# Performance work log

Hardware: AMD Instinct MI355X
Metric: run time of the kernel (lower is better)

## Reference

```python
import jax, jax.numpy as jnp
import numpy as np

E, NH, G = 2048, 16, 4
HD = E // NH          # head_dim = 128
KV = E // G           # kv proj width = 512 == G * HD
B, S = 2, 2048


def setup_inputs() -> dict:
    key = jax.random.key(0)
    ks = jax.random.split(key, 7)
    s = lambda n: 1.0 / np.sqrt(n)
    return {
        "query": jax.random.normal(ks[0], (B, S, E), jnp.float32),
        "key_in": jax.random.normal(ks[1], (B, S, E), jnp.float32),
        "value": jax.random.normal(ks[2], (B, S, E), jnp.float32),
        "Wq": jax.random.normal(ks[3], (E, E), jnp.float32) * s(E),
        "bq": jnp.zeros((E,), jnp.float32),
        "Wk": jax.random.normal(ks[4], (E, KV), jnp.float32) * s(E),
        "bk": jnp.zeros((KV,), jnp.float32),
        "Wv": jax.random.normal(ks[5], (E, KV), jnp.float32) * s(E),
        "bv": jnp.zeros((KV,), jnp.float32),
        "Wo": jax.random.normal(ks[6], (E, E), jnp.float32) * s(E),
        "bo": jnp.zeros((E,), jnp.float32),
    }


def reference(query, key_in, value, Wq, bq, Wk, bk, Wv, bv, Wo, bo):
    b, s, _ = query.shape
    scale = HD ** -0.5
    # projections
    q = (query @ Wq + bq).reshape(b, s, NH, HD).transpose(0, 2, 1, 3)   # [B,NH,S,HD]
    k = (key_in @ Wk + bk).reshape(b, s, G, HD).transpose(0, 2, 1, 3)   # [B,G,S,HD]
    v = (value @ Wv + bv).reshape(b, s, G, HD).transpose(0, 2, 1, 3)    # [B,G,S,HD]
    # grouped-query attention: each KV head serves NH//G query heads
    qg = q.reshape(b, G, NH // G, s, HD)                                # [B,G,NH/G,S,HD]
    scores = jnp.einsum('bgqsh,bgth->bgqst', qg, k) * scale             # [B,G,NH/G,S,S]
    w = jax.nn.softmax(scores, axis=-1)
    out = jnp.einsum('bgqst,bgth->bgqsh', w, v)                         # [B,G,NH/G,S,HD]
    out = out.reshape(b, NH, s, HD).transpose(0, 2, 1, 3).reshape(b, s, E)
    return out @ Wo + bo
```

## Files before the change

### kernel.cpp

```cpp
#include <hip/hip_runtime.h>
#include <hip/hip_bf16.h>

#define E_ 2048
#define S_ 2048
#define B_ 2
#define BS_ 4096
#define KV_ 512
#define NH_ 16
#define G_ 4
#define HD_ 128
#define QK_SCALE 0.08838834764831845f
#define LOG2E_ 1.4426950408889634f

typedef __attribute__((ext_vector_type(8))) short short8;
typedef __attribute__((ext_vector_type(4))) float floatx4;
typedef __attribute__((ext_vector_type(4))) unsigned short ushort4_;

static __device__ __forceinline__ unsigned short f2bf(float f) {
  unsigned int u = __builtin_bit_cast(unsigned int, f);
  u += 0x7fffu + ((u >> 16) & 1u);
  return (unsigned short)(u >> 16);
}

static __device__ __forceinline__ unsigned int cvt_pk_bf16(float lo, float hi) {
  unsigned int r;
  asm("v_cvt_pk_bf16_f32 %0, %1, %2" : "=v"(r) : "v"(lo), "v"(hi));
  return r;
}

static __device__ __forceinline__ void gld16(const void* g, void* l) {
  __builtin_amdgcn_global_load_lds(
      (const __attribute__((address_space(1))) unsigned int*)g,
      (__attribute__((address_space(3))) unsigned int*)l, 16, 0, 0);
}

__global__ __launch_bounds__(256) void k_prep(
    const float* __restrict__ q, const float* __restrict__ k, const float* __restrict__ v,
    unsigned short* __restrict__ xq, unsigned short* __restrict__ xk,
    unsigned short* __restrict__ xv,
    const float* __restrict__ Wq, unsigned short* __restrict__ WqT,
    const float* __restrict__ Wk, unsigned short* __restrict__ WkT,
    const float* __restrict__ Wv, unsigned short* __restrict__ WvT,
    const float* __restrict__ Wo, unsigned short* __restrict__ WoT) {
  __shared__ float ts[32][33];
  int bid = blockIdx.x;
  if (bid < 24576) {
    int which = bid >> 13;
    int i = (bid & 8191) * 256 + threadIdx.x;
    const float* in = (which == 0) ? q : (which == 1) ? k : v;
    unsigned short* out = (which == 0) ? xq : (which == 1) ? xk : xv;
    float4 vv = reinterpret_cast<const float4*>(in)[i];
    ushort4_ o;
    o.x = f2bf(vv.x); o.y = f2bf(vv.y); o.z = f2bf(vv.z); o.w = f2bf(vv.w);
    reinterpret_cast<ushort4_*>(out)[i] = o;
    return;
  }
  int t = bid - 24576;
  const float* in; unsigned short* out; int N; int rem;
  if (t < 4096)      { in = Wq; out = WqT; N = 2048; rem = t; }
  else if (t < 5120) { in = Wk; out = WkT; N = 512;  rem = t - 4096; }
  else if (t < 6144) { in = Wv; out = WvT; N = 512;  rem = t - 5120; }
  else               { in = Wo; out = WoT; N = 2048; rem = t - 6144; }
  const int K = 2048;
  int nx = N >> 5;
  int bx = rem % nx, by = rem / nx;
  int tx = threadIdx.x & 31, ty = threadIdx.x >> 5;
  int n0 = bx * 32, k0 = by * 32;
#pragma unroll
  for (int i = 0; i < 4; ++i)
    ts[ty + i * 8][tx] = in[(size_t)(k0 + ty + i * 8) * N + n0 + tx];
  __syncthreads();
#pragma unroll
  for (int i = 0; i < 4; ++i)
    out[(size_t)(n0 + ty + i * 8) * K + k0 + tx] = f2bf(ts[tx][ty + i * 8]);
}

template <bool OUT_F32>
static __device__ __forceinline__ void gemm_bt_tile(
    const unsigned short* __restrict__ A, const unsigned short* __restrict__ Bt,
    const float* __restrict__ bias, bool rowBias, void* __restrict__ C,
    int N, int K, float scale, int bx, int by,
    unsigned short* As, unsigned short* Bs) {
  const int tid = threadIdx.x;
  const int w = tid >> 6;
  const int lhi = (tid >> 4) & 3;
  const int llo = tid & 15;
  const int wr = w >> 1, wc = w & 1;
  const size_t brow = (size_t)by * 128, bcol = (size_t)bx * 128;

  auto stage = [&](int k0, int bufi) {
#pragma unroll
    for (int i = 0; i < 2; ++i) {
      int o = i * 256 + tid;
      gld16(A + (brow + (o >> 2)) * K + k0 + (o & 3) * 8,
            As + bufi * 4096 + (size_t)(i * 256 + w * 64) * 8);
      gld16(Bt + (bcol + (o >> 2)) * K + k0 + (o & 3) * 8,
            Bs + bufi * 4096 + (size_t)(i * 256 + w * 64) * 8);
    }
  };

  floatx4 acc[4][4];
#pragma unroll
  for (int i = 0; i < 4; ++i)
#pragma unroll
    for (int j = 0; j < 4; ++j)
      acc[i][j] = (floatx4){0.f, 0.f, 0.f, 0.f};

  stage(0, 0);
  __syncthreads();
  int buf = 0;
  const int nk = K >> 5;
  for (int t = 0; t < nk; ++t) {
    if (t + 1 < nk) stage((t + 1) * 32, buf ^ 1);
    const unsigned short* Ab = As + buf * 4096;
    const unsigned short* Bb = Bs + buf * 4096;
    short8 a[4], b[4];
#pragma unroll
    for (int f = 0; f < 4; ++f) {
      a[f] = *reinterpret_cast<const short8*>(Ab + (wr * 64 + f * 16 + llo) * 32 + lhi * 8);
      b[f] = *reinterpret_cast<const short8*>(Bb + (wc * 64 + f * 16 + llo) * 32 + lhi * 8);
    }
    __builtin_amdgcn_s_setprio(1);
#pragma unroll
    for (int i = 0; i < 4; ++i)
#pragma unroll
      for (int j = 0; j < 4; ++j)
        acc[i][j] = __builtin_amdgcn_mfma_f32_16x16x32_bf16(a[i], b[j], acc[i][j], 0, 0, 0);
    __builtin_amdgcn_s_setprio(0);
    __syncthreads();
    buf ^= 1;
  }

#pragma unroll
  for (int i = 0; i < 4; ++i) {
#pragma unroll
    for (int j = 0; j < 4; ++j) {
      size_t gr0 = brow + wr * 64 + i * 16 + lhi * 4;
      size_t gc = bcol + wc * 64 + j * 16 + llo;
#pragma unroll
      for (int r = 0; r < 4; ++r) {
        size_t grow = gr0 + r;
        float v = acc[i][j][r];
        v += rowBias ? bias[grow] : bias[gc];
        v *= scale;
        if (OUT_F32)
          ((float*)C)[grow * N + gc] = v;
        else
          ((unsigned short*)C)[grow * N + gc] = f2bf(v);
      }
    }
  }
}

__global__ __launch_bounds__(256) void k_gemm_qkv(
    const unsigned short* __restrict__ xq, const unsigned short* __restrict__ WqT,
    const float* __restrict__ bq, unsigned short* __restrict__ qb,
    const unsigned short* __restrict__ xk, const unsigned short* __restrict__ WkT,
    const float* __restrict__ bk, unsigned short* __restrict__ kb,
    const unsigned short* __restrict__ WvT, const unsigned short* __restrict__ xv,
    const float* __restrict__ bv, unsigned short* __restrict__ vtb) {
  __shared__ __align__(16) unsigned short As[2 * 128 * 32];
  __shared__ __align__(16) unsigned short Bs[2 * 128 * 32];
  int bid = blockIdx.x;
  if (bid < 512) {
    int cm = (bid & 7) * 64 + (bid >> 3);
    gemm_bt_tile<false>(xq, WqT, bq, false, qb, E_, E_, QK_SCALE * LOG2E_,
                        cm >> 5, cm & 31, As, Bs);
  } else if (bid < 640) {
    int u = bid - 512;
    int cm = (u & 7) * 16 + (u >> 3);
    gemm_bt_tile<false>(xk, WkT, bk, false, kb, KV_, E_, 1.0f, cm >> 5, cm & 31, As, Bs);
  } else {
    int u = bid - 640;
    int cm = (u & 7) * 16 + (u >> 3);
    gemm_bt_tile<false>(WvT, xv, bv, true, vtb, BS_, E_, 1.0f, cm >> 2, cm & 3, As, Bs);
  }
}

__global__ __launch_bounds__(256) void k_gemm_o(
    const unsigned short* __restrict__ A, const unsigned short* __restrict__ Bt,
    const float* __restrict__ bias, float* __restrict__ C) {
  __shared__ __align__(16) unsigned short As[2 * 128 * 32];
  __shared__ __align__(16) unsigned short Bs[2 * 128 * 32];
  int cm = (blockIdx.x & 7) * 64 + (blockIdx.x >> 3);
  gemm_bt_tile<true>(A, Bt, bias, false, C, E_, E_, 1.0f, cm >> 5, cm & 31, As, Bs);
}

__global__ __launch_bounds__(512) void k_attn(
    const unsigned short* __restrict__ qb, const unsigned short* __restrict__ kb,
    const unsigned short* __restrict__ vt, unsigned short* __restrict__ attn) {
  __shared__ __align__(16) unsigned short Ks[2][64 * 128];
  __shared__ __align__(16) unsigned short Vs[2][128 * 64];
  __shared__ __align__(16) unsigned short Ps[8][32 * 64];

  const int tid = threadIdx.x;
  const int w = tid >> 6;
  const int lhi = (tid >> 4) & 3;
  const int llo = tid & 15;
  const int bid = blockIdx.x;
  const int xcd = bid & 7;
  const int b = xcd >> 2, g = xcd & 3;
  const int inner = bid >> 3;
  const int hq = inner & 3, qt = inner >> 2;
  const int h = g * 4 + hq;

  char* PsW = (char*)&Ps[0][0] + w * 4096;

  short8 qf[2][4];
#pragma unroll
  for (int rt = 0; rt < 2; ++rt)
#pragma unroll
    for (int hc = 0; hc < 4; ++hc) {
      int row = qt * 256 + w * 32 + rt * 16 + llo;
      qf[rt][hc] = *reinterpret_cast<const short8*>(
          qb + ((size_t)(b * 2048 + row)) * 2048 + h * 128 + hc * 32 + lhi * 8);
    }

  floatx4 acc[2][8];
#pragma unroll
  for (int rt = 0; rt < 2; ++rt)
#pragma unroll
    for (int dc = 0; dc < 8; ++dc)
      acc[rt][dc] = (floatx4){0.f, 0.f, 0.f, 0.f};
  float m_[2] = {-1e30f, -1e30f};
  float l_[2] = {0.f, 0.f};

  auto stage = [&](int kv0, int buf) {
#pragma unroll
    for (int i = 0; i < 2; ++i) {
      int o = i * 512 + tid;
      int row = o >> 4, gr2 = (o & 15) ^ (row & 7);
      gld16(kb + ((size_t)(b * 2048 + kv0 + row)) * 512 + g * 128 + gr2 * 8,
            &Ks[buf][(size_t)(i * 512 + w * 64) * 8]);
    }
#pragma unroll
    for (int i = 0; i < 2; ++i) {
      int o = i * 512 + tid;
      int row = o >> 3, gr2 = (o & 7) ^ (row & 7);
      gld16(vt + ((size_t)(g * 128 + row)) * 4096 + b * 2048 + kv0 + gr2 * 8,
            &Vs[buf][(size_t)(i * 512 + w * 64) * 8]);
    }
  };

  stage(0, 0);
  __syncthreads();
  int buf = 0;

  for (int t = 0; t < 32; ++t) {
    const int kv0 = t * 64;
    if (t < 31) stage(kv0 + 64, buf ^ 1);

    floatx4 sc[2][4];
#pragma unroll
    for (int rt = 0; rt < 2; ++rt)
#pragma unroll
      for (int c = 0; c < 4; ++c)
        sc[rt][c] = (floatx4){0.f, 0.f, 0.f, 0.f};
    __builtin_amdgcn_s_setprio(1);
#pragma unroll
    for (int c = 0; c < 4; ++c) {
      int krow = c * 16 + llo;
#pragma unroll
      for (int hc = 0; hc < 4; ++hc) {
        int byteoff = krow * 256 + ((hc * 64 + lhi * 16) ^ ((krow & 7) << 4));
        short8 kf = *reinterpret_cast<const short8*>((const char*)&Ks[buf][0] + byteoff);
        sc[0][c] = __builtin_amdgcn_mfma_f32_16x16x32_bf16(kf, qf[0][hc], sc[0][c], 0, 0, 0);
        sc[1][c] = __builtin_amdgcn_mfma_f32_16x16x32_bf16(kf, qf[1][hc], sc[1][c], 0, 0, 0);
      }
    }
    __builtin_amdgcn_s_setprio(0);

#pragma unroll
    for (int rt = 0; rt < 2; ++rt) {
      float pm = sc[rt][0][0];
#pragma unroll
      for (int c = 0; c < 4; ++c)
#pragma unroll
        for (int r = 0; r < 4; ++r) pm = fmaxf(pm, sc[rt][c][r]);
      if (__any(pm > m_[rt] + 8.0f)) {
        float t2 = pm;
        t2 = fmaxf(t2, __shfl_xor(t2, 16));
        t2 = fmaxf(t2, __shfl_xor(t2, 32));
        float m2 = fmaxf(m_[rt], t2);
        float scr = __builtin_amdgcn_exp2f(m_[rt] - m2);
        m_[rt] = m2;
        l_[rt] *= scr;
#pragma unroll
        for (int r = 0; r < 4; ++r) {
          float s_r = __shfl(scr, (tid & 48) | (((tid >> 2) & 12) + r));
#pragma unroll
          for (int dc = 0; dc < 8; ++dc) acc[rt][dc][r] *= s_r;
        }
      }
      float lsum = l_[rt];
#pragma unroll
      for (int c = 0; c < 4; ++c) {
        float e0 = __builtin_amdgcn_exp2f(sc[rt][c][0] - m_[rt]);
        float e1 = __builtin_amdgcn_exp2f(sc[rt][c][1] - m_[rt]);
        float e2 = __builtin_amdgcn_exp2f(sc[rt][c][2] - m_[rt]);
        float e3 = __builtin_amdgcn_exp2f(sc[rt][c][3] - m_[rt]);
        lsum += (e0 + e1) + (e2 + e3);
        uint2 pk;
        pk.x = cvt_pk_bf16(e0, e1);
        pk.y = cvt_pk_bf16(e2, e3);
        int byteoff = (rt * 16 + llo) * 128 + ((c * 32 + lhi * 8) ^ ((llo & 7) << 4));
        *reinterpret_cast<uint2*>(PsW + byteoff) = pk;
      }
      l_[rt] = lsum;
    }

    short8 pf[2][2];
#pragma unroll
    for (int rt = 0; rt < 2; ++rt)
#pragma unroll
      for (int kc = 0; kc < 2; ++kc) {
        int byteoff = (rt * 16 + llo) * 128 + ((kc * 64 + lhi * 16) ^ ((llo & 7) << 4));
        pf[rt][kc] = *reinterpret_cast<const short8*>(PsW + byteoff);
      }
    __builtin_amdgcn_s_setprio(1);
#pragma unroll
    for (int dc = 0; dc < 8; ++dc) {
      int vrow = dc * 16 + llo;
      int bo0 = vrow * 128 + ((lhi * 16) ^ ((vrow & 7) << 4));
      int bo1 = vrow * 128 + ((64 + lhi * 16) ^ ((vrow & 7) << 4));
      short8 vf0 = *reinterpret_cast<const short8*>((const char*)&Vs[buf][0] + bo0);
      short8 vf1 = *reinterpret_cast<const short8*>((const char*)&Vs[buf][0] + bo1);
      acc[0][dc] = __builtin_amdgcn_mfma_f32_16x16x32_bf16(pf[0][0], vf0, acc[0][dc], 0, 0, 0);
      acc[1][dc] = __builtin_amdgcn_mfma_f32_16x16x32_bf16(pf[1][0], vf0, acc[1][dc], 0, 0, 0);
      acc[0][dc] = __builtin_amdgcn_mfma_f32_16x16x32_bf16(pf[0][1], vf1, acc[0][dc], 0, 0, 0);
      acc[1][dc] = __builtin_amdgcn_mfma_f32_16x16x32_bf16(pf[1][1], vf1, acc[1][dc], 0, 0, 0);
    }
    __builtin_amdgcn_s_setprio(0);
    __syncthreads();
    buf ^= 1;
  }

#pragma unroll
  for (int rt = 0; rt < 2; ++rt) {
    float t2 = l_[rt];
    t2 += __shfl_xor(t2, 16);
    t2 += __shfl_xor(t2, 32);
    float linv = 1.0f / t2;
    float lr[4];
#pragma unroll
    for (int r = 0; r < 4; ++r)
      lr[r] = __shfl(linv, (tid & 48) | (((tid >> 2) & 12) + r));
#pragma unroll
    for (int dc = 0; dc < 8; ++dc)
#pragma unroll
      for (int r = 0; r < 4; ++r) {
        int row = qt * 256 + w * 32 + rt * 16 + lhi * 4 + r;
        float v = acc[rt][dc][r] * lr[r];
        attn[((size_t)(b * 2048 + row)) * 2048 + h * 128 + dc * 16 + llo] = f2bf(v);
      }
  }
}

extern "C" void kernel_launch(void* const* d_in, const int* in_sizes, int n_in,
                              void* d_out, int out_size, void* d_ws, size_t ws_size,
                              hipStream_t stream) {
  const float* query  = (const float*)d_in[0];
  const float* key_in = (const float*)d_in[1];
  const float* value  = (const float*)d_in[2];
  const float* Wq = (const float*)d_in[3];
  const float* bq = (const float*)d_in[4];
  const float* Wk = (const float*)d_in[5];
  const float* bk = (const float*)d_in[6];
  const float* Wv = (const float*)d_in[7];
  const float* bv = (const float*)d_in[8];
  const float* Wo = (const float*)d_in[9];
  const float* bo = (const float*)d_in[10];
  float* out = (float*)d_out;

  char* ws = (char*)d_ws;
  size_t off = 0;
  auto alloc = [&](size_t bytes) {
    char* p = ws + off;
    off += (bytes + 255) & ~(size_t)255;
    return p;
  };
  unsigned short* xq   = (unsigned short*)alloc((size_t)BS_ * E_ * 2);
  unsigned short* xk   = (unsigned short*)alloc((size_t)BS_ * E_ * 2);
  unsigned short* xv   = (unsigned short*)alloc((size_t)BS_ * E_ * 2);
  unsigned short* WqT  = (unsigned short*)alloc((size_t)E_ * E_ * 2);
  unsigned short* WkT  = (unsigned short*)alloc((size_t)KV_ * E_ * 2);
  unsigned short* WvT  = (unsigned short*)alloc((size_t)KV_ * E_ * 2);
  unsigned short* WoT  = (unsigned short*)alloc((size_t)E_ * E_ * 2);
  unsigned short* qb   = (unsigned short*)alloc((size_t)BS_ * E_ * 2);
  unsigned short* kb   = (unsigned short*)alloc((size_t)BS_ * KV_ * 2);
  unsigned short* vtb  = (unsigned short*)alloc((size_t)KV_ * BS_ * 2);
  unsigned short* attb = (unsigned short*)alloc((size_t)BS_ * E_ * 2);

  k_prep<<<34816, 256, 0, stream>>>(query, key_in, value, xq, xk, xv,
                                    Wq, WqT, Wk, WkT, Wv, WvT, Wo, WoT);
  k_gemm_qkv<<<768, 256, 0, stream>>>(xq, WqT, bq, qb, xk, WkT, bk, kb,
                                      WvT, xv, bv, vtb);
  k_attn<<<B_ * NH_ * (S_ / 256), 512, 0, stream>>>(qb, kb, vtb, attb);
  k_gemm_o<<<512, 256, 0, stream>>>(attb, WoT, bo, out);
}
```

Measured before the change: 247.1 us.

## Fuse fp32-to-bf16 activation conversion into QKV GEMM tile loads

Removes the separate pass that converts query/key/value activations to bf16 in the prep kernel. The QKV GEMM now reads fp32 activations directly with register loads, packs them to bf16 with v_cvt_pk_bf16, and writes them into LDS. This saves a full read and write of three activation tensors through a workspace. In exchange, those operands lose the async global_load_lds path, so loads go through registers and the GEMM re-reads the fp32 activations (twice the bytes) once per column tile.

```diff
diff --git a/kernel.cpp b/kernel.cpp
--- a/kernel.cpp
+++ b/kernel.cpp
@@ -35,27 +35,12 @@
 }
 
 __global__ __launch_bounds__(256) void k_prep(
-    const float* __restrict__ q, const float* __restrict__ k, const float* __restrict__ v,
-    unsigned short* __restrict__ xq, unsigned short* __restrict__ xk,
-    unsigned short* __restrict__ xv,
     const float* __restrict__ Wq, unsigned short* __restrict__ WqT,
     const float* __restrict__ Wk, unsigned short* __restrict__ WkT,
     const float* __restrict__ Wv, unsigned short* __restrict__ WvT,
     const float* __restrict__ Wo, unsigned short* __restrict__ WoT) {
   __shared__ float ts[32][33];
-  int bid = blockIdx.x;
-  if (bid < 24576) {
-    int which = bid >> 13;
-    int i = (bid & 8191) * 256 + threadIdx.x;
-    const float* in = (which == 0) ? q : (which == 1) ? k : v;
-    unsigned short* out = (which == 0) ? xq : (which == 1) ? xk : xv;
-    float4 vv = reinterpret_cast<const float4*>(in)[i];
-    ushort4_ o;
-    o.x = f2bf(vv.x); o.y = f2bf(vv.y); o.z = f2bf(vv.z); o.w = f2bf(vv.w);
-    reinterpret_cast<ushort4_*>(out)[i] = o;
-    return;
-  }
-  int t = bid - 24576;
+  int t = blockIdx.x;
   const float* in; unsigned short* out; int N; int rem;
   if (t < 4096)      { in = Wq; out = WqT; N = 2048; rem = t; }
   else if (t < 5120) { in = Wk; out = WkT; N = 512;  rem = t - 4096; }
@@ -75,9 +60,9 @@
     out[(size_t)(n0 + ty + i * 8) * K + k0 + tx] = f2bf(ts[tx][ty + i * 8]);
 }
 
-template <bool OUT_F32>
+template <bool OUT_F32, bool A_F32, bool B_F32>
 static __device__ __forceinline__ void gemm_bt_tile(
-    const unsigned short* __restrict__ A, const unsigned short* __restrict__ Bt,
+    const void* __restrict__ A, const void* __restrict__ Bt,
     const float* __restrict__ bias, bool rowBias, void* __restrict__ C,
     int N, int K, float scale, int bx, int by,
     unsigned short* As, unsigned short* Bs) {
@@ -92,10 +77,30 @@
 #pragma unroll
     for (int i = 0; i < 2; ++i) {
       int o = i * 256 + tid;
-      gld16(A + (brow + (o >> 2)) * K + k0 + (o & 3) * 8,
-            As + bufi * 4096 + (size_t)(i * 256 + w * 64) * 8);
-      gld16(Bt + (bcol + (o >> 2)) * K + k0 + (o & 3) * 8,
-            Bs + bufi * 4096 + (size_t)(i * 256 + w * 64) * 8);
+      if constexpr (A_F32) {
+        int row = o >> 2, gcol = o & 3;
+        const float4* src = reinterpret_cast<const float4*>(
+            (const float*)A + (brow + row) * (size_t)K + k0 + gcol * 8);
+        float4 v0 = src[0], v1 = src[1];
+        uint4 pk = {cvt_pk_bf16(v0.x, v0.y), cvt_pk_bf16(v0.z, v0.w),
+                    cvt_pk_bf16(v1.x, v1.y), cvt_pk_bf16(v1.z, v1.w)};
+        *reinterpret_cast<uint4*>(As + bufi * 4096 + (size_t)o * 8) = pk;
+      } else {
+        gld16((const unsigned short*)A + (brow + (o >> 2)) * (size_t)K + k0 + (o & 3) * 8,
+              As + bufi * 4096 + (size_t)(i * 256 + w * 64) * 8);
+      }
+      if constexpr (B_F32) {
+        int row = o >> 2, gcol = o & 3;
+        const float4* src = reinterpret_cast<const float4*>(
+            (const float*)Bt + (bcol + row) * (size_t)K + k0 + gcol * 8);
+        float4 v0 = src[0], v1 = src[1];
+        uint4 pk = {cvt_pk_bf16(v0.x, v0.y), cvt_pk_bf16(v0.z, v0.w),
+                    cvt_pk_bf16(v1.x, v1.y), cvt_pk_bf16(v1.z, v1.w)};
+        *reinterpret_cast<uint4*>(Bs + bufi * 4096 + (size_t)o * 8) = pk;
+      } else {
+        gld16((const unsigned short*)Bt + (bcol + (o >> 2)) * (size_t)K + k0 + (o & 3) * 8,
+              Bs + bufi * 4096 + (size_t)(i * 256 + w * 64) * 8);
+      }
     }
   };
 
@@ -153,27 +158,29 @@
 }
 
 __global__ __launch_bounds__(256) void k_gemm_qkv(
-    const unsigned short* __restrict__ xq, const unsigned short* __restrict__ WqT,
+    const float* __restrict__ query, const unsigned short* __restrict__ WqT,
     const float* __restrict__ bq, unsigned short* __restrict__ qb,
-    const unsigned short* __restrict__ xk, const unsigned short* __restrict__ WkT,
+    const float* __restrict__ key_in, const unsigned short* __restrict__ WkT,
     const float* __restrict__ bk, unsigned short* __restrict__ kb,
-    const unsigned short* __restrict__ WvT, const unsigned short* __restrict__ xv,
+    const unsigned short* __restrict__ WvT, const float* __restrict__ value,
     const float* __restrict__ bv, unsigned short* __restrict__ vtb) {
   __shared__ __align__(16) unsigned short As[2 * 128 * 32];
   __shared__ __align__(16) unsigned short Bs[2 * 128 * 32];
   int bid = blockIdx.x;
   if (bid < 512) {
     int cm = (bid & 7) * 64 + (bid >> 3);
-    gemm_bt_tile<false>(xq, WqT, bq, false, qb, E_, E_, QK_SCALE * LOG2E_,
-                        cm >> 5, cm & 31, As, Bs);
+    gemm_bt_tile<false, true, false>(query, WqT, bq, false, qb, E_, E_,
+                                     QK_SCALE * LOG2E_, cm >> 5, cm & 31, As, Bs);
   } else if (bid < 640) {
     int u = bid - 512;
     int cm = (u & 7) * 16 + (u >> 3);
-    gemm_bt_tile<false>(xk, WkT, bk, false, kb, KV_, E_, 1.0f, cm >> 5, cm & 31, As, Bs);
+    gemm_bt_tile<false, true, false>(key_in, WkT, bk, false, kb, KV_, E_, 1.0f,
+                                     cm >> 5, cm & 31, As, Bs);
   } else {
     int u = bid - 640;
     int cm = (u & 7) * 16 + (u >> 3);
-    gemm_bt_tile<false>(WvT, xv, bv, true, vtb, BS_, E_, 1.0f, cm >> 2, cm & 3, As, Bs);
+    gemm_bt_tile<false, false, true>(WvT, value, bv, true, vtb, BS_, E_, 1.0f,
+                                     cm >> 2, cm & 3, As, Bs);
   }
 }
 
@@ -183,7 +190,8 @@
   __shared__ __align__(16) unsigned short As[2 * 128 * 32];
   __shared__ __align__(16) unsigned short Bs[2 * 128 * 32];
   int cm = (blockIdx.x & 7) * 64 + (blockIdx.x >> 3);
-  gemm_bt_tile<true>(A, Bt, bias, false, C, E_, E_, 1.0f, cm >> 5, cm & 31, As, Bs);
+  gemm_bt_tile<true, false, false>(A, Bt, bias, false, C, E_, E_, 1.0f,
+                                   cm >> 5, cm & 31, As, Bs);
 }
 
 __global__ __launch_bounds__(512) void k_attn(
@@ -379,9 +387,6 @@
     off += (bytes + 255) & ~(size_t)255;
     return p;
   };
-  unsigned short* xq   = (unsigned short*)alloc((size_t)BS_ * E_ * 2);
-  unsigned short* xk   = (unsigned short*)alloc((size_t)BS_ * E_ * 2);
-  unsigned short* xv   = (unsigned short*)alloc((size_t)BS_ * E_ * 2);
   unsigned short* WqT  = (unsigned short*)alloc((size_t)E_ * E_ * 2);
   unsigned short* WkT  = (unsigned short*)alloc((size_t)KV_ * E_ * 2);
   unsigned short* WvT  = (unsigned short*)alloc((size_t)KV_ * E_ * 2);
@@ -391,10 +396,9 @@
   unsigned short* vtb  = (unsigned short*)alloc((size_t)KV_ * BS_ * 2);
   unsigned short* attb = (unsigned short*)alloc((size_t)BS_ * E_ * 2);
 
-  k_prep<<<34816, 256, 0, stream>>>(query, key_in, value, xq, xk, xv,
-                                    Wq, WqT, Wk, WkT, Wv, WvT, Wo, WoT);
-  k_gemm_qkv<<<768, 256, 0, stream>>>(xq, WqT, bq, qb, xk, WkT, bk, kb,
-                                      WvT, xv, bv, vtb);
+  k_prep<<<10240, 256, 0, stream>>>(Wq, WqT, Wk, WkT, Wv, WvT, Wo, WoT);
+  k_gemm_qkv<<<768, 256, 0, stream>>>(query, WqT, bq, qb, key_in, WkT, bk, kb,
+                                      WvT, value, bv, vtb);
   k_attn<<<B_ * NH_ * (S_ / 256), 512, 0, stream>>>(qb, kb, vtb, attb);
   k_gemm_o<<<512, 256, 0, stream>>>(attb, WoT, bo, out);
 }
```

Result: faster. 227.8 us (-7.8%).
